# Performance work log

Hardware: AMD Instinct MI355X
Metric: run time of the kernel (lower is better)

## Reference

```python
import jax, jax.numpy as jnp
import numpy as np

D_MODEL = 1024
NUM_HEADS = 16
HEAD_DIM = D_MODEL // NUM_HEADS  # 64
SEQ = 2048
BATCH = 4
LN_EPS = 1e-5


def setup_inputs() -> dict:
    key = jax.random.key(0)
    k_in, k_qkv, k_o, k_g = jax.random.split(key, 4)
    inputs = jax.random.normal(k_in, (BATCH, SEQ, D_MODEL), dtype=jnp.float32)
    mask = jnp.zeros((BATCH, 1, SEQ, SEQ), dtype=jnp.float32)  # additive mask
    # Realistic rotary embeddings (RoPE), duplicated-halves layout
    inv_freq = 1.0 / (10000.0 ** (jnp.arange(0, HEAD_DIM, 2, dtype=jnp.float32) / HEAD_DIM))
    pos = jnp.arange(SEQ, dtype=jnp.float32)
    freqs = pos[:, None] * inv_freq[None, :]            # [S, Dh/2]
    emb = jnp.concatenate([freqs, freqs], axis=-1)       # [S, Dh]
    cos = jnp.cos(emb)
    sin = jnp.sin(emb)
    # Parameters
    sd = 1.0 / np.sqrt(D_MODEL)
    w_qkv = jax.random.normal(k_qkv, (D_MODEL, 3 * D_MODEL), dtype=jnp.float32) * sd
    w_o = jax.random.normal(k_o, (D_MODEL, D_MODEL), dtype=jnp.float32) * sd
    ln_gamma = jnp.ones((D_MODEL,), dtype=jnp.float32)
    return {"inputs": inputs, "mask": mask, "cos": cos, "sin": sin,
            "ln_gamma": ln_gamma, "w_qkv": w_qkv, "w_o": w_o}


def _rotate_half(x):
    x1, x2 = jnp.split(x, 2, axis=-1)
    return jnp.concatenate([-x2, x1], axis=-1)


def reference(inputs, mask, cos, sin, ln_gamma, w_qkv, w_o):
    B, S, D = inputs.shape
    # Pre-attention LayerNorm (layer_id != 0), center=False -> no beta
    mu = jnp.mean(inputs, axis=-1, keepdims=True)
    var = jnp.mean(jnp.square(inputs - mu), axis=-1, keepdims=True)
    x = (inputs - mu) / jnp.sqrt(var + LN_EPS) * ln_gamma
    # Fused QKV projection, split into heads: [B, H, S, Dh]
    qkv = (x @ w_qkv).reshape(B, S, 3, NUM_HEADS, HEAD_DIM)
    qkv = jnp.transpose(qkv, (2, 0, 3, 1, 4))
    q, k, v = qkv[0], qkv[1], qkv[2]
    # RoPE
    c = cos.reshape(1, 1, S, HEAD_DIM)
    s = sin.reshape(1, 1, S, HEAD_DIM)
    q = q * c + _rotate_half(q) * s
    k = k * c + _rotate_half(k) * s
    # Scaled dot-product attention with additive mask
    scale = 1.0 / jnp.sqrt(jnp.asarray(HEAD_DIM, dtype=q.dtype))
    logits = jnp.einsum("bhqd,bhkd->bhqk", q, k) * scale + mask
    attn = jax.nn.softmax(logits, axis=-1)
    out = jnp.einsum("bhqk,bhkd->bhqd", attn, v)
    out = jnp.transpose(out, (0, 2, 1, 3)).reshape(B, S, D)
    return out @ w_o
```

## Files before the change

### kernel.cpp

```cpp
#include <hip/hip_runtime.h>
#include <stdint.h>

#define DEV __device__ __forceinline__

typedef __bf16 bf16x8 __attribute__((ext_vector_type(8)));
typedef float f32x4 __attribute__((ext_vector_type(4)));
typedef float f32x16 __attribute__((ext_vector_type(16)));

DEV unsigned short f2bf(float f) {
  union { float f; uint32_t u; } c; c.f = f;
  uint32_t u = c.u;
  u += 0x7FFFu + ((u >> 16) & 1u);
  return (unsigned short)(u >> 16);
}
DEV float bf2f(unsigned short h) {
  union { uint32_t u; float f; } c; c.u = ((uint32_t)h) << 16;
  return c.f;
}
DEV float u2f(uint32_t u) {
  union { uint32_t u; float f; } c; c.u = u;
  return c.f;
}
DEV bf16x8 ld8(const unsigned short* p) {
  uint4 u = *reinterpret_cast<const uint4*>(p);
  return __builtin_bit_cast(bf16x8, u);
}
DEV uint32_t cvtpk(float lo, float hi) {
  uint32_t r;
  asm("v_cvt_pk_bf16_f32 %0, %1, %2" : "=v"(r) : "v"(lo), "v"(hi));
  return r;
}
DEV void permswap(uint32_t& a, uint32_t& b) {
  asm("v_permlane32_swap_b32 %0, %1" : "+v"(a), "+v"(b));
}
DEV float exp2b(float x) { return __builtin_amdgcn_exp2f(x); }
DEV void gload16(const void* g, void* l) {
  __builtin_amdgcn_global_load_lds((const __attribute__((address_space(1))) void*)g,
                                   (__attribute__((address_space(3))) void*)l, 16, 0, 0);
}

template<int K, int N>
__global__ __launch_bounds__(256)
void transpose_cast_kernel(const float* __restrict__ in, unsigned short* __restrict__ out) {
  __shared__ float tile[64][65];
  const int bk = blockIdx.x % (K / 64);
  const int bn = blockIdx.x / (K / 64);
  const int k0 = bk * 64, n0 = bn * 64;
  const int t = threadIdx.x;
#pragma unroll
  for (int i = 0; i < 16; ++i) {
    int idx = t + i * 256;
    int kl = idx >> 6, nl = idx & 63;
    tile[kl][nl] = in[(size_t)(k0 + kl) * N + n0 + nl];
  }
  __syncthreads();
#pragma unroll
  for (int i = 0; i < 16; ++i) {
    int idx = t + i * 256;
    int nl = idx >> 6, kl = idx & 63;
    out[(size_t)(n0 + nl) * K + k0 + kl] = f2bf(tile[kl][nl]);
  }
}

__global__ __launch_bounds__(256)
void ln_kernel(const float* __restrict__ x, const float* __restrict__ gamma,
               unsigned short* __restrict__ y) {
  const int row = blockIdx.x;
  const int t = threadIdx.x;
  const float4 v = reinterpret_cast<const float4*>(x + (size_t)row * 1024)[t];
  float s  = v.x + v.y + v.z + v.w;
  float s2 = v.x * v.x + v.y * v.y + v.z * v.z + v.w * v.w;
#pragma unroll
  for (int off = 1; off < 64; off <<= 1) {
    s  += __shfl_xor(s, off);
    s2 += __shfl_xor(s2, off);
  }
  __shared__ float red[8];
  const int w = t >> 6, lane = t & 63;
  if (lane == 0) { red[w] = s; red[4 + w] = s2; }
  __syncthreads();
  s  = red[0] + red[1] + red[2] + red[3];
  s2 = red[4] + red[5] + red[6] + red[7];
  const float mu = s * (1.0f / 1024.0f);
  const float var = s2 * (1.0f / 1024.0f) - mu * mu;
  const float rstd = rsqrtf(var + 1e-5f);
  const float4 g = reinterpret_cast<const float4*>(gamma)[t];
  ushort4 o;
  o.x = f2bf((v.x - mu) * rstd * g.x);
  o.y = f2bf((v.y - mu) * rstd * g.y);
  o.z = f2bf((v.z - mu) * rstd * g.z);
  o.w = f2bf((v.w - mu) * rstd * g.w);
  reinterpret_cast<ushort4*>(y + (size_t)row * 1024)[t] = o;
}

template<int N_DIM, bool OUT_F32>
__global__ __launch_bounds__(256)
void gemm_bt_kernel(const unsigned short* __restrict__ A,
                    const unsigned short* __restrict__ Bt,
                    void* __restrict__ Cout) {
  constexpr int K = 1024;
  __shared__ unsigned short a_lds[128 * 32];
  __shared__ unsigned short b_lds[128 * 32];
  const int t = threadIdx.x;
  const int w = t >> 6, l = t & 63;
  const int lrow = l & 15, lch = l >> 4;
  const int nbn = N_DIM / 128;
  const int m0 = (blockIdx.x / nbn) * 128;
  const int n0 = (blockIdx.x % nbn) * 128;
  const int wm = (w >> 1) * 64, wn = (w & 1) * 64;

  const int srow = t >> 2;
  const int schk = t & 3;
  const int scol = ((schk ^ (srow & 3)) << 3);
  const unsigned short* aS0 = A  + (size_t)(m0 + srow) * K + scol;
  const unsigned short* aS1 = A  + (size_t)(m0 + 64 + srow) * K + scol;
  const unsigned short* bS0 = Bt + (size_t)(n0 + srow) * K + scol;
  const unsigned short* bS1 = Bt + (size_t)(n0 + 64 + srow) * K + scol;
  unsigned short* aD0 = a_lds + (w * 16) * 32;
  unsigned short* aD1 = a_lds + (64 + w * 16) * 32;
  unsigned short* bD0 = b_lds + (w * 16) * 32;
  unsigned short* bD1 = b_lds + (64 + w * 16) * 32;

  f32x4 acc[4][4] = {};

  for (int k0 = 0; k0 < K; k0 += 32) {
    gload16(aS0 + k0, aD0);
    gload16(aS1 + k0, aD1);
    gload16(bS0 + k0, bD0);
    gload16(bS1 + k0, bD1);
    __syncthreads();
    bf16x8 af[4], bfr[4];
#pragma unroll
    for (int m = 0; m < 4; ++m) {
      int row = wm + m * 16 + lrow;
      af[m] = ld8(a_lds + row * 32 + ((lch ^ (lrow & 3)) << 3));
    }
#pragma unroll
    for (int n = 0; n < 4; ++n) {
      int row = wn + n * 16 + lrow;
      bfr[n] = ld8(b_lds + row * 32 + ((lch ^ (lrow & 3)) << 3));
    }
#pragma unroll
    for (int m = 0; m < 4; ++m)
#pragma unroll
      for (int n = 0; n < 4; ++n)
        acc[m][n] = __builtin_amdgcn_mfma_f32_16x16x32_bf16(af[m], bfr[n], acc[m][n], 0, 0, 0);
    __syncthreads();
  }

#pragma unroll
  for (int m = 0; m < 4; ++m) {
    const int grow0 = m0 + wm + m * 16 + lch * 4;
#pragma unroll
    for (int n = 0; n < 4; ++n) {
      const int gcol = n0 + wn + n * 16 + lrow;
#pragma unroll
      for (int r = 0; r < 4; ++r) {
        if constexpr (OUT_F32)
          ((float*)Cout)[(size_t)(grow0 + r) * N_DIM + gcol] = acc[m][n][r];
        else
          ((unsigned short*)Cout)[(size_t)(grow0 + r) * N_DIM + gcol] = f2bf(acc[m][n][r]);
      }
    }
  }
}

__global__ __launch_bounds__(256)
void rope_split_kernel(const unsigned short* __restrict__ qkv,
                       const float* __restrict__ cosb,
                       const float* __restrict__ sinb,
                       unsigned short* __restrict__ Qo,
                       unsigned short* __restrict__ Kf,
                       unsigned short* __restrict__ Vf) {
  const int bid = blockIdx.x;
  const int sb = bid & 31, h = (bid >> 5) & 15, b = bid >> 9;
  const int s0 = sb * 64;
  const int t = threadIdx.x;
  __shared__ unsigned short qt[64][72], kt[64][72], vt[64][72];

  const int sl = t >> 2, c0 = (t & 3) * 16;
  {
    const size_t base = (size_t)(b * 2048 + s0 + sl) * 3072 + h * 64 + c0;
    uint4 q1 = *(const uint4*)(qkv + base);
    uint4 q2 = *(const uint4*)(qkv + base + 8);
    uint4 k1 = *(const uint4*)(qkv + base + 1024);
    uint4 k2 = *(const uint4*)(qkv + base + 1032);
    uint4 v1 = *(const uint4*)(qkv + base + 2048);
    uint4 v2 = *(const uint4*)(qkv + base + 2056);
    *(uint4*)&qt[sl][c0] = q1; *(uint4*)&qt[sl][c0 + 8] = q2;
    *(uint4*)&kt[sl][c0] = k1; *(uint4*)&kt[sl][c0 + 8] = k2;
    *(uint4*)&vt[sl][c0] = v1; *(uint4*)&vt[sl][c0 + 8] = v2;
  }
  __syncthreads();
  const size_t fbase = (size_t)(b * 16 + h) * 131072;
  {
    const int sg = s0 + sl;
    alignas(16) unsigned short qo16[16], ko16[16];
#pragma unroll
    for (int j = 0; j < 16; ++j) {
      const int d = c0 + j;
      const float cv = cosb[sg * 64 + d], sv = sinb[sg * 64 + d];
      const float qv = bf2f(qt[sl][d]), qp = bf2f(qt[sl][d ^ 32]);
      const float kv = bf2f(kt[sl][d]), kp = bf2f(kt[sl][d ^ 32]);
      const float rq = qv * cv + ((d < 32) ? -qp : qp) * sv;
      const float rk = kv * cv + ((d < 32) ? -kp : kp) * sv;
      qo16[j] = f2bf(rq * 0.180336880f);
      ko16[j] = f2bf(rk);
    }
    const size_t ob = ((size_t)(b * 16 + h) * 2048 + sg) * 64 + c0;
    *(uint4*)(Qo + ob) = *(uint4*)qo16; *(uint4*)(Qo + ob + 8) = *(uint4*)(qo16 + 8);
    unsigned short* kd = Kf + fbase + ((size_t)((sb * 2 + (sl >> 5)) * 4 + (t & 3))) * 512;
    *(uint4*)(kd + (sl & 31) * 8)        = *(uint4*)ko16;
    *(uint4*)(kd + (32 + (sl & 31)) * 8) = *(uint4*)(ko16 + 8);
  }
  {
    const int dh = t >> 2, sc0 = (t & 3) * 16;
    alignas(16) unsigned short vo16[16];
#pragma unroll
    for (int j = 0; j < 16; ++j) vo16[j] = vt[sc0 + j][dh];
    unsigned short* vd = Vf + fbase + ((size_t)((sb * 2 + (dh >> 5)) * 4 + (t & 3))) * 512;
    *(uint4*)(vd + (dh & 31) * 8)        = *(uint4*)vo16;
    *(uint4*)(vd + (32 + (dh & 31)) * 8) = *(uint4*)(vo16 + 8);
  }
}

__global__ __launch_bounds__(256)
void mask_prep_kernel(const float* __restrict__ mask, unsigned short* __restrict__ mrs,
                      unsigned char* __restrict__ flg) {
  const int bid = blockIdx.x;
  const int kvt = bid & 31, qc = (bid >> 5) & 31, b = bid >> 10;
  const int t = threadIdx.x;
  __shared__ float tile[64][72];
  __shared__ int nzf;
  if (t == 0) nzf = 0;
  uint32_t orbits = 0;
  {
    const int r = t >> 2, c0 = (t & 3) * 16;
    const float* src = mask + (size_t)b * (2048ull * 2048) + (size_t)(qc * 64 + r) * 2048 + kvt * 64 + c0;
#pragma unroll
    for (int i = 0; i < 4; ++i) {
      const float4 v = *(const float4*)(src + i * 4);
      *(float4*)&tile[r][c0 + i * 4] = v;
      orbits |= __float_as_uint(v.x) | __float_as_uint(v.y) |
                __float_as_uint(v.z) | __float_as_uint(v.w);
    }
  }
  __syncthreads();
  if (orbits != 0u) nzf = 1;
  __syncthreads();
  if (nzf) {
    const int cid = t >> 5;
    const int n = cid >> 2, jj = (cid >> 1) & 1, hi = cid & 1;
    const int qq0 = (t & 31) * 2;
    const int cb = n * 32 + jj * 16 + hi * 4;
    unsigned short* dst = mrs + (((size_t)(b * 32 + kvt) * 8 + cid) * 2048 + qc * 64) * 8;
#pragma unroll
    for (int qo = 0; qo < 2; ++qo) {
      const int q = qq0 + qo;
      alignas(16) unsigned short o8[8];
#pragma unroll
      for (int v = 0; v < 8; ++v) {
        const int col = cb + (v >> 2) * 8 + (v & 3);
        o8[v] = f2bf(tile[q][col] * 1.44269504f);
      }
      *(uint4*)(dst + (size_t)q * 8) = *(uint4*)o8;
    }
  }
  if (t == 0) flg[(size_t)(b * 32 + kvt) * 32 + qc] = (unsigned char)nzf;
}

__global__ __launch_bounds__(256)
void attn_kernel(const unsigned short* __restrict__ Q,
                 const unsigned short* __restrict__ Kf,
                 const unsigned short* __restrict__ Vf,
                 const unsigned short* __restrict__ mrs,
                 const unsigned char* __restrict__ flg,
                 unsigned short* __restrict__ O) {
  const int t = threadIdx.x, w = t >> 6, l = t & 63;
  const int lq = l & 31, hi = l >> 5;
  const int bid = blockIdx.x;
  const int x = bid & 7, y = bid >> 3;
  const int bh = x * 8 + (y >> 4);
  const int qb = y & 15;
  const int b = bh >> 4, h = bh & 15;
  const int q0 = qb * 128 + w * 32;

  const unsigned short* Qb  = Q  + (size_t)bh * (2048 * 64);
  const unsigned short* Kfb = Kf + (size_t)bh * 131072 + l * 8;
  const unsigned short* Vfb = Vf + (size_t)bh * 131072 + l * 8;
  const unsigned short* ml = mrs + (size_t)b * 4194304 + (size_t)hi * 16384 + (size_t)(q0 + lq) * 8;
  const unsigned char* fb = flg + (size_t)(b * 32) * 32 + qb * 2;

  __shared__ unsigned short k_lds[2][4096];
  __shared__ unsigned short v_lds[2][4096];

  bf16x8 qf[4];
  {
    const unsigned short* qp = Qb + (size_t)(q0 + lq) * 64 + hi * 8;
#pragma unroll
    for (int c = 0; c < 4; ++c) qf[c] = ld8(qp + c * 16);
  }
  bf16x8 ones;
  {
    const uint4 ou = { 0x3F803F80u, 0x3F803F80u, 0x3F803F80u, 0x3F803F80u };
    ones = __builtin_bit_cast(bf16x8, ou);
  }

  f32x16 ot0 = {}, ot1 = {};
  f32x16 st_sum = {};
  int cur = 0;

  unsigned int bmap = 0;
  for (int kvt = 0; kvt < 32; ++kvt)
    if (fb[kvt * 32] | fb[kvt * 32 + 1]) bmap |= (1u << kvt);

  const int ch0 = w * 2;
  gload16(Kfb + (size_t)(ch0)     * 512, k_lds[0] + (ch0)     * 512);
  gload16(Kfb + (size_t)(ch0 + 1) * 512, k_lds[0] + (ch0 + 1) * 512);
  gload16(Vfb + (size_t)(ch0)     * 512, v_lds[0] + (ch0)     * 512);
  gload16(Vfb + (size_t)(ch0 + 1) * 512, v_lds[0] + (ch0 + 1) * 512);
  __syncthreads();

  for (int kvt = 0; kvt < 32; ++kvt) {
    const bool hm = (bmap >> kvt) & 1u;
    if (kvt + 1 < 32) {
      const unsigned short* kS = Kfb + (size_t)(kvt + 1) * 4096;
      const unsigned short* vS = Vfb + (size_t)(kvt + 1) * 4096;
      unsigned short* kD = k_lds[cur ^ 1];
      unsigned short* vD = v_lds[cur ^ 1];
      gload16(kS + (size_t)(ch0)     * 512, kD + (ch0)     * 512);
      gload16(kS + (size_t)(ch0 + 1) * 512, kD + (ch0 + 1) * 512);
      gload16(vS + (size_t)(ch0)     * 512, vD + (ch0)     * 512);
      gload16(vS + (size_t)(ch0 + 1) * 512, vD + (ch0 + 1) * 512);
    }

    const unsigned short* kb = k_lds[cur] + l * 8;
    const unsigned short* vb = v_lds[cur] + l * 8;
    bf16x8 kfr[8], vfr[8];
#pragma unroll
    for (int i = 0; i < 8; ++i) kfr[i] = ld8(kb + i * 512);
#pragma unroll
    for (int i = 0; i < 8; ++i) vfr[i] = ld8(vb + i * 512);

    f32x16 st0 = {}, st1 = {};
    if (hm) {
      const unsigned short* mp = ml + (size_t)kvt * 131072;
      uint4 mc[4];
#pragma unroll
      for (int c2 = 0; c2 < 4; ++c2) mc[c2] = *(const uint4*)(mp + c2 * 32768);
#pragma unroll
      for (int jj = 0; jj < 2; ++jj) {
        const uint4 u0 = mc[jj];
        const uint4 u1 = mc[2 + jj];
#pragma unroll
        for (int wv = 0; wv < 4; ++wv) {
          const uint32_t w0 = ((const uint32_t*)&u0)[wv];
          const uint32_t w1 = ((const uint32_t*)&u1)[wv];
          st0[jj * 8 + wv * 2]     = u2f(w0 << 16);
          st0[jj * 8 + wv * 2 + 1] = u2f(w0 & 0xffff0000u);
          st1[jj * 8 + wv * 2]     = u2f(w1 << 16);
          st1[jj * 8 + wv * 2 + 1] = u2f(w1 & 0xffff0000u);
        }
      }
    }

    __builtin_amdgcn_s_setprio(1);
#pragma unroll
    for (int c = 0; c < 4; ++c) {
      st0 = __builtin_amdgcn_mfma_f32_32x32x16_bf16(kfr[c],     qf[c], st0, 0, 0, 0);
      st1 = __builtin_amdgcn_mfma_f32_32x32x16_bf16(kfr[4 + c], qf[c], st1, 0, 0, 0);
    }
    __builtin_amdgcn_s_setprio(0);

#pragma unroll
    for (int r = 0; r < 16; ++r) {
      st0[r] = exp2b(st0[r]);
      st1[r] = exp2b(st1[r]);
    }

    bf16x8 pa[4];
#pragma unroll
    for (int c = 0; c < 4; ++c) {
      const int e8 = (c & 1) * 8;
      uint32_t A01, B01, A23, B23;
      if (c < 2) {
        A01 = cvtpk(st0[e8 + 0], st0[e8 + 1]);
        B01 = cvtpk(st0[e8 + 4], st0[e8 + 5]);
        A23 = cvtpk(st0[e8 + 2], st0[e8 + 3]);
        B23 = cvtpk(st0[e8 + 6], st0[e8 + 7]);
      } else {
        A01 = cvtpk(st1[e8 + 0], st1[e8 + 1]);
        B01 = cvtpk(st1[e8 + 4], st1[e8 + 5]);
        A23 = cvtpk(st1[e8 + 2], st1[e8 + 3]);
        B23 = cvtpk(st1[e8 + 6], st1[e8 + 7]);
      }
      permswap(A01, B01);
      permswap(A23, B23);
      const uint4 pw = { A01, A23, B01, B23 };
      pa[c] = __builtin_bit_cast(bf16x8, pw);
    }

    __builtin_amdgcn_s_setprio(1);
#pragma unroll
    for (int c = 0; c < 4; ++c) {
      ot0 = __builtin_amdgcn_mfma_f32_32x32x16_bf16(vfr[c],     pa[c], ot0, 0, 0, 0);
      ot1 = __builtin_amdgcn_mfma_f32_32x32x16_bf16(vfr[4 + c], pa[c], ot1, 0, 0, 0);
      st_sum = __builtin_amdgcn_mfma_f32_32x32x16_bf16(ones, pa[c], st_sum, 0, 0, 0);
    }
    __builtin_amdgcn_s_setprio(0);

    __syncthreads();
    cur ^= 1;
  }

  const float inv = 1.0f / st_sum[0];
  unsigned short* ob = O + ((size_t)(b * 2048 + q0 + lq) * 16 + h) * 64 + hi * 4;
#pragma unroll
  for (int td = 0; td < 2; ++td) {
#pragma unroll
    for (int rr = 0; rr < 4; ++rr) {
      ushort4 ov;
      if (td == 0) {
        ov.x = f2bf(ot0[rr * 4 + 0] * inv);
        ov.y = f2bf(ot0[rr * 4 + 1] * inv);
        ov.z = f2bf(ot0[rr * 4 + 2] * inv);
        ov.w = f2bf(ot0[rr * 4 + 3] * inv);
      } else {
        ov.x = f2bf(ot1[rr * 4 + 0] * inv);
        ov.y = f2bf(ot1[rr * 4 + 1] * inv);
        ov.z = f2bf(ot1[rr * 4 + 2] * inv);
        ov.w = f2bf(ot1[rr * 4 + 3] * inv);
      }
      *(ushort4*)(ob + td * 32 + rr * 8) = ov;
    }
  }
}

extern "C" void kernel_launch(void* const* d_in, const int* in_sizes, int n_in,
                              void* d_out, int out_size, void* d_ws, size_t ws_size,
                              hipStream_t stream) {
  (void)in_sizes; (void)n_in; (void)out_size; (void)ws_size;
  const float* x     = (const float*)d_in[0];
  const float* mask  = (const float*)d_in[1];
  const float* cosb  = (const float*)d_in[2];
  const float* sinb  = (const float*)d_in[3];
  const float* gamma = (const float*)d_in[4];
  const float* w_qkv = (const float*)d_in[5];
  const float* w_o   = (const float*)d_in[6];

  char* ws = (char*)d_ws;
  unsigned short* x_bf   = (unsigned short*)(ws);
  unsigned short* wqkvT  = (unsigned short*)(ws + 16777216);
  unsigned short* woT    = (unsigned short*)(ws + 23068672);
  unsigned short* qkv_bf = (unsigned short*)(ws + 25165824);
  unsigned short* q_r    = (unsigned short*)(ws + 75497472);
  unsigned short* k_f    = (unsigned short*)(ws + 92274688);
  unsigned short* v_f    = (unsigned short*)(ws + 109051904);
  unsigned short* attn   = (unsigned short*)(ws + 125829120);
  unsigned short* mask_rs = qkv_bf;
  unsigned char*  flags   = (unsigned char*)(ws + 25165824 + 33554432);

  transpose_cast_kernel<1024, 3072><<<dim3(16 * 48), dim3(256), 0, stream>>>(w_qkv, wqkvT);
  transpose_cast_kernel<1024, 1024><<<dim3(16 * 16), dim3(256), 0, stream>>>(w_o, woT);
  ln_kernel<<<dim3(8192), dim3(256), 0, stream>>>(x, gamma, x_bf);
  gemm_bt_kernel<3072, false><<<dim3(64 * 24), dim3(256), 0, stream>>>(x_bf, wqkvT, (void*)qkv_bf);
  rope_split_kernel<<<dim3(4 * 16 * 32), dim3(256), 0, stream>>>(qkv_bf, cosb, sinb, q_r, k_f, v_f);
  mask_prep_kernel<<<dim3(4096), dim3(256), 0, stream>>>(mask, mask_rs, flags);
  attn_kernel<<<dim3(1024), dim3(256), 0, stream>>>(q_r, k_f, v_f, mask_rs, flags, attn);
  gemm_bt_kernel<1024, true><<<dim3(64 * 8), dim3(256), 0, stream>>>(attn, woT, d_out);
}
```

Baseline: 251.3 us.

## Prefetch K/V tiles through registers and interleave LDS reads with MFMAs

Replaces the direct global-to-LDS async loads (gload16) with register prefetch. The next K/V tile is loaded into VGPRs early in each iteration and written to the other LDS buffer after the QK and softmax phase, and the barrier moves to the top of the loop. K and V fragments are now read from LDS just before each MFMA rather than all up front, which lowers register pressure. The aim is to hide global latency behind compute and cut VGPR usage, at the cost of extra VGPRs for the prefetch, explicit LDS stores, and LDS reads placed on the MFMA critical path.

```diff
diff --git a/kernel.cpp b/kernel.cpp
--- a/kernel.cpp
+++ b/kernel.cpp
@@ -285,9 +285,9 @@
   const int b = bh >> 4, h = bh & 15;
   const int q0 = qb * 128 + w * 32;
 
-  const unsigned short* Qb  = Q  + (size_t)bh * (2048 * 64);
-  const unsigned short* Kfb = Kf + (size_t)bh * 131072 + l * 8;
-  const unsigned short* Vfb = Vf + (size_t)bh * 131072 + l * 8;
+  const unsigned short* Qb = Q  + (size_t)bh * (2048 * 64);
+  const unsigned short* Ks = Kf + (size_t)bh * 131072 + t * 16;
+  const unsigned short* Vs = Vf + (size_t)bh * 131072 + t * 16;
   const unsigned short* ml = mrs + (size_t)b * 4194304 + (size_t)hi * 16384 + (size_t)(q0 + lq) * 8;
   const unsigned char* fb = flg + (size_t)(b * 32) * 32 + qb * 2;
 
@@ -314,33 +314,27 @@
   for (int kvt = 0; kvt < 32; ++kvt)
     if (fb[kvt * 32] | fb[kvt * 32 + 1]) bmap |= (1u << kvt);
 
-  const int ch0 = w * 2;
-  gload16(Kfb + (size_t)(ch0)     * 512, k_lds[0] + (ch0)     * 512);
-  gload16(Kfb + (size_t)(ch0 + 1) * 512, k_lds[0] + (ch0 + 1) * 512);
-  gload16(Vfb + (size_t)(ch0)     * 512, v_lds[0] + (ch0)     * 512);
-  gload16(Vfb + (size_t)(ch0 + 1) * 512, v_lds[0] + (ch0 + 1) * 512);
-  __syncthreads();
+  uint4 ka0 = *(const uint4*)Ks;
+  uint4 ka1 = *(const uint4*)(Ks + 8);
+  uint4 va0 = *(const uint4*)Vs;
+  uint4 va1 = *(const uint4*)(Vs + 8);
+  *(uint4*)(k_lds[0] + t * 16)     = ka0;
+  *(uint4*)(k_lds[0] + t * 16 + 8) = ka1;
+  *(uint4*)(v_lds[0] + t * 16)     = va0;
+  *(uint4*)(v_lds[0] + t * 16 + 8) = va1;
 
   for (int kvt = 0; kvt < 32; ++kvt) {
+    __syncthreads();
     const bool hm = (bmap >> kvt) & 1u;
-    if (kvt + 1 < 32) {
-      const unsigned short* kS = Kfb + (size_t)(kvt + 1) * 4096;
-      const unsigned short* vS = Vfb + (size_t)(kvt + 1) * 4096;
-      unsigned short* kD = k_lds[cur ^ 1];
-      unsigned short* vD = v_lds[cur ^ 1];
-      gload16(kS + (size_t)(ch0)     * 512, kD + (ch0)     * 512);
-      gload16(kS + (size_t)(ch0 + 1) * 512, kD + (ch0 + 1) * 512);
-      gload16(vS + (size_t)(ch0)     * 512, vD + (ch0)     * 512);
-      gload16(vS + (size_t)(ch0 + 1) * 512, vD + (ch0 + 1) * 512);
-    }
-
-    const unsigned short* kb = k_lds[cur] + l * 8;
-    const unsigned short* vb = v_lds[cur] + l * 8;
-    bf16x8 kfr[8], vfr[8];
-#pragma unroll
-    for (int i = 0; i < 8; ++i) kfr[i] = ld8(kb + i * 512);
-#pragma unroll
-    for (int i = 0; i < 8; ++i) vfr[i] = ld8(vb + i * 512);
+    const bool more = (kvt + 1) < 32;
+    if (more) {
+      const unsigned short* kS = Ks + (size_t)(kvt + 1) * 4096;
+      const unsigned short* vS = Vs + (size_t)(kvt + 1) * 4096;
+      ka0 = *(const uint4*)kS;
+      ka1 = *(const uint4*)(kS + 8);
+      va0 = *(const uint4*)vS;
+      va1 = *(const uint4*)(vS + 8);
+    }
 
     f32x16 st0 = {}, st1 = {};
     if (hm) {
@@ -364,11 +358,14 @@
       }
     }
 
+    const unsigned short* kb = k_lds[cur] + l * 8;
     __builtin_amdgcn_s_setprio(1);
 #pragma unroll
     for (int c = 0; c < 4; ++c) {
-      st0 = __builtin_amdgcn_mfma_f32_32x32x16_bf16(kfr[c],     qf[c], st0, 0, 0, 0);
-      st1 = __builtin_amdgcn_mfma_f32_32x32x16_bf16(kfr[4 + c], qf[c], st1, 0, 0, 0);
+      const bf16x8 kf0 = ld8(kb + c * 512);
+      const bf16x8 kf1 = ld8(kb + (4 + c) * 512);
+      st0 = __builtin_amdgcn_mfma_f32_32x32x16_bf16(kf0, qf[c], st0, 0, 0, 0);
+      st1 = __builtin_amdgcn_mfma_f32_32x32x16_bf16(kf1, qf[c], st1, 0, 0, 0);
     }
     __builtin_amdgcn_s_setprio(0);
 
@@ -400,16 +397,26 @@
       pa[c] = __builtin_bit_cast(bf16x8, pw);
     }
 
+    if (more) {
+      unsigned short* kn = k_lds[cur ^ 1] + t * 16;
+      unsigned short* vn = v_lds[cur ^ 1] + t * 16;
+      *(uint4*)kn       = ka0;
+      *(uint4*)(kn + 8) = ka1;
+      *(uint4*)vn       = va0;
+      *(uint4*)(vn + 8) = va1;
+    }
+
+    const unsigned short* vb = v_lds[cur] + l * 8;
     __builtin_amdgcn_s_setprio(1);
 #pragma unroll
     for (int c = 0; c < 4; ++c) {
-      ot0 = __builtin_amdgcn_mfma_f32_32x32x16_bf16(vfr[c],     pa[c], ot0, 0, 0, 0);
-      ot1 = __builtin_amdgcn_mfma_f32_32x32x16_bf16(vfr[4 + c], pa[c], ot1, 0, 0, 0);
+      const bf16x8 vf0 = ld8(vb + c * 512);
+      const bf16x8 vf1 = ld8(vb + (4 + c) * 512);
+      ot0 = __builtin_amdgcn_mfma_f32_32x32x16_bf16(vf0, pa[c], ot0, 0, 0, 0);
+      ot1 = __builtin_amdgcn_mfma_f32_32x32x16_bf16(vf1, pa[c], ot1, 0, 0, 0);
       st_sum = __builtin_amdgcn_mfma_f32_32x32x16_bf16(ones, pa[c], st_sum, 0, 0, 0);
     }
     __builtin_amdgcn_s_setprio(0);
-
-    __syncthreads();
     cur ^= 1;
   }
 
```

Result: faster. 243.1 us (-3.2%).
